# Kernel optimization log

Hardware: AMD Instinct MI355X
Metric: run time of the kernel (lower is better)

The kernel has to match this reference:

```python
import jax, jax.numpy as jnp
import numpy as np

N = 8192      # total nodes
B = 64        # graphs in batch
NPG = 128     # nodes per graph (equal-size graphs; idx sorted)
D_IN = 256
H = 256       # hidden_dim (d_model)
NH = 4        # nhead
HD = H // NH
FF = 2 * H    # dim_feedforward
NC = 16       # n_class


def setup_inputs() -> dict:
    key = jax.random.key(0)
    ks = jax.random.split(key, 16)
    def rn(k, shp, scale=0.05):
        return jax.random.normal(k, shp, jnp.float32) * scale
    inp = {}
    inp["x_in"] = jax.random.normal(ks[0], (N, D_IN), jnp.float32)
    # scale adjacency so each row sums ~1 to keep activations well-conditioned
    inp["adj"] = jax.random.uniform(ks[1], (N, N), jnp.float32) * (2.0 / N)
    inp["idx"] = jnp.repeat(jnp.arange(B, dtype=jnp.int32), NPG)
    inp["cum_nodes"] = jnp.full((B,), NPG, jnp.int32)
    # fc1
    inp["W1"] = rn(ks[2], (D_IN, H)); inp["b1"] = jnp.zeros((H,), jnp.float32)
    # transformer encoder layer (eval mode, dropout inactive)
    inp["in_w"] = rn(ks[3], (H, 3 * H)); inp["in_b"] = jnp.zeros((3 * H,), jnp.float32)
    inp["out_w"] = rn(ks[4], (H, H));    inp["out_b"] = jnp.zeros((H,), jnp.float32)
    inp["ln1_s"] = jnp.ones((H,), jnp.float32); inp["ln1_b"] = jnp.zeros((H,), jnp.float32)
    inp["ff1_w"] = rn(ks[5], (H, FF)); inp["ff1_b"] = jnp.zeros((FF,), jnp.float32)
    inp["ff2_w"] = rn(ks[6], (FF, H)); inp["ff2_b"] = jnp.zeros((H,), jnp.float32)
    inp["ln2_s"] = jnp.ones((H,), jnp.float32); inp["ln2_b"] = jnp.zeros((H,), jnp.float32)
    # fc3 / fc4
    inp["W3"] = rn(ks[7], (H, H));  inp["b3"] = jnp.zeros((H,), jnp.float32)
    inp["W4"] = rn(ks[8], (H, NC)); inp["b4"] = jnp.zeros((NC,), jnp.float32)
    return inp


def _layer_norm(x, s, b):
    mu = x.mean(-1, keepdims=True)
    xc = x - mu
    return xc * jax.lax.rsqrt((xc * xc).mean(-1, keepdims=True) + 1e-5) * s + b


def reference(x_in, adj, idx, cum_nodes, W1, b1, in_w, in_b, out_w, out_b,
              ln1_s, ln1_b, ff1_w, ff1_b, ff2_w, ff2_b, ln2_s, ln2_b,
              W3, b3, W4, b4):
    Bg = cum_nodes.shape[0]
    n = x_in.shape[0] // Bg  # equal-size graphs -> pad_sequence == reshape
    x = x_in @ W1 + b1                      # fc1
    x = jax.nn.relu(adj @ x)                # adjacency message passing
    p = x.reshape(Bg, n, H)                 # pack: idx is sorted, graphs equal size
    # --- TransformerEncoderLayer (post-LN, relu FFN, eval mode) ---
    qkv = p @ in_w + in_b                   # [B, n, 3H]
    q, k, v = jnp.split(qkv, 3, axis=-1)
    q = q.reshape(Bg, n, NH, HD); k = k.reshape(Bg, n, NH, HD); v = v.reshape(Bg, n, NH, HD)
    att = jax.nn.softmax(jnp.einsum('bqhd,bkhd->bhqk', q, k) / np.sqrt(HD), axis=-1)
    o = jnp.einsum('bhqk,bkhd->bqhd', att, v).reshape(Bg, n, H) @ out_w + out_b
    y = _layer_norm(p + o, ln1_s, ln1_b)
    ff = jax.nn.relu(y @ ff1_w + ff1_b) @ ff2_w + ff2_b
    y = _layer_norm(y + ff, ln2_s, ln2_b)
    # --- unpack + scatter-add pooling over graphs ---
    flat = y.reshape(Bg * n, H)
    pooled = jax.ops.segment_sum(flat, idx, num_segments=Bg)  # [B, H]
    out = jax.nn.relu(pooled @ W3 + b3) @ W4 + b4
    return jax.nn.log_softmax(out, axis=-1)
```

## Files before the change

### kernel.cpp

```cpp
#include <hip/hip_runtime.h>

typedef float fx4 __attribute__((ext_vector_type(4)));
typedef short s16x8 __attribute__((ext_vector_type(8)));
typedef short s16x4 __attribute__((ext_vector_type(4)));
typedef unsigned short ushort_t;

__device__ __forceinline__ short f2bf(float f) {
  union { float f; unsigned u; } v; v.f = f;
  unsigned r = v.u + 0x7FFFu + ((v.u >> 16) & 1u);
  return (short)(r >> 16);
}

__device__ __forceinline__ float bf2f(short h) {
  union { float f; unsigned u; } v;
  v.u = ((unsigned)(unsigned short)h) << 16;
  return v.f;
}

__device__ __forceinline__ unsigned cvt_pk_bf16(float a, float b) {
  unsigned r;
  asm("v_cvt_pk_bf16_f32 %0, %1, %2" : "=v"(r) : "v"(a), "v"(b));
  return r;
}

__device__ __forceinline__ s16x8 cvt8(fx4 a, fx4 b) {
  union { s16x8 s; unsigned u[4]; } w;
  w.u[0] = cvt_pk_bf16(a[0], a[1]);
  w.u[1] = cvt_pk_bf16(a[2], a[3]);
  w.u[2] = cvt_pk_bf16(b[0], b[1]);
  w.u[3] = cvt_pk_bf16(b[2], b[3]);
  return w.s;
}

__device__ __forceinline__ void gload16(const void* g, void* l) {
  __builtin_amdgcn_global_load_lds(
      (const __attribute__((address_space(1))) unsigned int*)g,
      (__attribute__((address_space(3))) unsigned int*)l, 16, 0, 0);
}

__global__ __launch_bounds__(256) void prep_kernel(
    const float* __restrict__ W1, const float* __restrict__ in_w,
    const float* __restrict__ out_w, const float* __restrict__ ff1_w,
    const float* __restrict__ ff2_w,
    ushort_t* __restrict__ W1t, ushort_t* __restrict__ in_wT,
    ushort_t* __restrict__ out_wT, ushort_t* __restrict__ ff1t,
    ushort_t* __restrict__ ff2t) {
  const int bid = blockIdx.x, t = threadIdx.x;
  const float* W; ushort_t* Wt; int K, N, base;
  if (bid < 256)       { W = W1;    Wt = W1t;    K = 256; N = 256; base = 0; }
  else if (bid < 1024) { W = in_w;  Wt = in_wT;  K = 256; N = 768; base = 256; }
  else if (bid < 1280) { W = out_w; Wt = out_wT; K = 256; N = 256; base = 1024; }
  else if (bid < 1792) { W = ff1_w; Wt = ff1t;   K = 256; N = 512; base = 1280; }
  else                 { W = ff2_w; Wt = ff2t;   K = 512; N = 256; base = 1792; }
  const int idx = (bid - base) * 256 + t;
  const int k = idx / N, n = idx - k * N;
  Wt[(size_t)n * K + k] = (ushort_t)f2bf(W[idx]);
}

template<int MF, bool AF32, int OUTM, bool RELU, bool RES>
__global__ __launch_bounds__(256) void gemm2(
    const void* __restrict__ Av, const ushort_t* __restrict__ Bt,
    const float* __restrict__ bias, const float* __restrict__ res,
    const float* __restrict__ lns, const float* __restrict__ lnb,
    float* __restrict__ Cf, ushort_t* __restrict__ Cb,
    int M, int N, int K, int kLen) {
  constexpr int BM = MF * 16;
  __shared__ __align__(16) ushort_t Asm[2][BM * 64];
  __shared__ __align__(16) ushort_t Bsm[256 * 64];
  const int t = threadIdx.x, lane = t & 63, wave = t >> 6;
  const int bm = blockIdx.y * BM;
  const int bn = blockIdx.x * 256;
  const int wn = wave * 64, fr = lane & 15, fq = lane >> 4;
  const int NT = kLen >> 6;
  const int x0 = ((fq) ^ (fr & 7)) * 8;
  const int x1 = ((4 + fq) ^ (fr & 7)) * 8;
  fx4 acc[MF][4] = {};

  const int gl = lane >> 3, gc = lane & 7;
  const int gsw = (gc ^ gl) * 8;
  const ushort_t* Bgl = Bt + (size_t)(bn + wave * 64 + gl) * K + gsw;
  const ushort_t* Agl =
      (const ushort_t*)Av + (size_t)(bm + wave * (BM / 4) + gl) * K + gsw;
  constexpr int TPR = 256 / BM;
  const int arow = t / TPR;
  const int ac0 = (t % TPR) * (BM / 4);
  const float* Afp = (const float*)Av + (size_t)(bm + arow) * K + ac0;
  fx4 R[MF / 2][2];

  auto issueB = [&](int kt) {
    #pragma unroll
    for (int i = 0; i < 8; ++i)
      gload16(Bgl + (size_t)i * 8 * K + kt * 64, &Bsm[wave * 4096 + i * 512]);
  };
  auto issueAg = [&](int buf, int kt) {
    #pragma unroll
    for (int i = 0; i < MF / 2; ++i)
      gload16(Agl + (size_t)i * 8 * K + kt * 64,
              &Asm[buf][wave * (BM * 16) + i * 512]);
  };
  auto loadR = [&](int kt) {
    #pragma unroll
    for (int w = 0; w < MF / 2; ++w) {
      R[w][0] = *(const fx4*)(Afp + kt * 64 + w * 8);
      R[w][1] = *(const fx4*)(Afp + kt * 64 + w * 8 + 4);
    }
  };
  auto writeA = [&](int buf) {
    #pragma unroll
    for (int w = 0; w < MF / 2; ++w) {
      const int cs = ((ac0 >> 3) + w) ^ (arow & 7);
      *(s16x8*)&Asm[buf][arow * 64 + cs * 8] = cvt8(R[w][0], R[w][1]);
    }
  };

  if constexpr (AF32) { loadR(0); issueB(0); writeA(0); loadR(1); }
  else { issueAg(0, 0); issueB(0); }
  __syncthreads();

  #pragma unroll 1
  for (int kt = 0; kt < NT; ++kt) {
    const int cur = kt & 1;
    s16x8 b0[4], b1[4], a0[MF], a1[MF];
    #pragma unroll
    for (int nf = 0; nf < 4; ++nf) {
      b0[nf] = *(const s16x8*)&Bsm[(wn + nf * 16 + fr) * 64 + x0];
      b1[nf] = *(const s16x8*)&Bsm[(wn + nf * 16 + fr) * 64 + x1];
    }
    #pragma unroll
    for (int mf = 0; mf < MF; ++mf)
      a0[mf] = *(const s16x8*)&Asm[cur][(mf * 16 + fr) * 64 + x0];
    asm volatile("s_waitcnt lgkmcnt(0)" ::: "memory");
    if (kt + 1 < NT) {
      if constexpr (AF32) {
        writeA(cur ^ 1);
        if (kt + 2 < NT) loadR(kt + 2);
        issueB(kt + 1);
      } else {
        issueAg(cur ^ 1, kt + 1);
        issueB(kt + 1);
      }
    }
    #pragma unroll
    for (int mf = 0; mf < MF; ++mf)
      #pragma unroll
      for (int nf = 0; nf < 4; ++nf)
        acc[mf][nf] = __builtin_amdgcn_mfma_f32_16x16x32_bf16(
            a0[mf], b0[nf], acc[mf][nf], 0, 0, 0);
    #pragma unroll
    for (int mf = 0; mf < MF; ++mf)
      a1[mf] = *(const s16x8*)&Asm[cur][(mf * 16 + fr) * 64 + x1];
    #pragma unroll
    for (int mf = 0; mf < MF; ++mf)
      #pragma unroll
      for (int nf = 0; nf < 4; ++nf)
        acc[mf][nf] = __builtin_amdgcn_mfma_f32_16x16x32_bf16(
            a1[mf], b1[nf], acc[mf][nf], 0, 0, 0);
    __syncthreads();
  }

  if constexpr (OUTM == 3) {
    #pragma unroll
    for (int mf = 0; mf < MF; ++mf)
      #pragma unroll
      for (int nf = 0; nf < 4; ++nf) {
        const int col = bn + wn + nf * 16 + fr;
        const float bb = bias[col];
        s16x4 w;
        #pragma unroll
        for (int r = 0; r < 4; ++r) w[r] = f2bf(acc[mf][nf][r] + bb);
        *(s16x4*)&Cb[(size_t)col * M + bm + mf * 16 + fq * 4] = w;
      }
  } else {
    #pragma unroll
    for (int mf = 0; mf < MF; ++mf)
      #pragma unroll
      for (int nf = 0; nf < 4; ++nf) {
        const int col = bn + wn + nf * 16 + fr;
        const float bb = bias[col];
        #pragma unroll
        for (int r = 0; r < 4; ++r) {
          const int row = bm + mf * 16 + fq * 4 + r;
          float x = acc[mf][nf][r] + bb;
          if constexpr (RES) x += res[(size_t)row * N + col];
          if constexpr (RELU) x = fmaxf(x, 0.f);
          if constexpr (OUTM == 0 || OUTM == 2) Cf[(size_t)row * N + col] = x;
          if constexpr (OUTM == 1 || OUTM == 2)
            Cb[(size_t)row * N + col] = (ushort_t)f2bf(x);
        }
      }
  }
}

__global__ __launch_bounds__(256) void adjmm6(
    const float* __restrict__ adj, const ushort_t* __restrict__ xT,
    ushort_t* __restrict__ part) {
  constexpr int NT = 16;
  __shared__ __align__(16) ushort_t Asm[2][128 * 64];
  __shared__ __align__(16) ushort_t Bsm[256 * 64];
  const int t = threadIdx.x, lane = t & 63, wave = t >> 6;
  const int kh = blockIdx.x, bm = blockIdx.y * 128;
  const int kOff = kh * 1024;
  const int wn = wave * 64, fr = lane & 15, fq = lane >> 4;
  const int x0 = (fq ^ (fr & 7)) * 8, x1 = ((4 + fq) ^ (fr & 7)) * 8;
  const int gl = lane >> 3, gsw = ((lane & 7) ^ gl) * 8;

  const ushort_t* Bgl = xT + (size_t)(wn + gl) * 8192 + kOff + gsw;
  const int arow = t >> 1;
  const int alane = t & 1;
  const float* Afp = adj + (size_t)(bm + arow) * 8192 + kOff;

  fx4 R[8];
  auto loadR = [&](int kt) {
    #pragma unroll
    for (int j = 0; j < 8; ++j)
      R[j] = *(const fx4*)(Afp + kt * 64 + alane * 4 + j * 8);
  };
  auto writeA = [&](int buf) {
    #pragma unroll
    for (int j = 0; j < 8; ++j) {
      union { s16x4 s; unsigned u[2]; } w;
      w.u[0] = cvt_pk_bf16(R[j][0], R[j][1]);
      w.u[1] = cvt_pk_bf16(R[j][2], R[j][3]);
      *(s16x4*)&Asm[buf][arow * 64 + (j ^ (arow & 7)) * 8 + alane * 4] = w.s;
    }
  };
  auto issueB = [&](int kt) {
    #pragma unroll
    for (int i = 0; i < 8; ++i)
      gload16(Bgl + (size_t)i * 8 * 8192 + kt * 64,
              &Bsm[wave * 4096 + i * 512]);
  };

  fx4 acc[8][4] = {};
  loadR(0);
  issueB(0);
  writeA(0);
  loadR(1);
  asm volatile("s_waitcnt lgkmcnt(0)" ::: "memory");
  asm volatile("s_waitcnt vmcnt(8)" ::: "memory");
  __builtin_amdgcn_sched_barrier(0);
  __builtin_amdgcn_s_barrier();
  __builtin_amdgcn_sched_barrier(0);

  #pragma unroll 1
  for (int kt = 0; kt < NT; ++kt) {
    const int cur = kt & 1;
    s16x8 b0[4], b1[4], a[8];
    #pragma unroll
    for (int nf = 0; nf < 4; ++nf) {
      b0[nf] = *(const s16x8*)&Bsm[(wn + nf * 16 + fr) * 64 + x0];
      b1[nf] = *(const s16x8*)&Bsm[(wn + nf * 16 + fr) * 64 + x1];
    }
    #pragma unroll
    for (int mf = 0; mf < 8; ++mf)
      a[mf] = *(const s16x8*)&Asm[cur][(mf * 16 + fr) * 64 + x0];
    asm volatile("s_waitcnt lgkmcnt(0)" ::: "memory");
    __builtin_amdgcn_sched_barrier(0);
    if (kt + 1 < NT) {
      issueB(kt + 1);
      writeA(cur ^ 1);
      if (kt + 2 < NT) loadR(kt + 2);
    }
    #pragma unroll
    for (int mf = 0; mf < 8; ++mf)
      #pragma unroll
      for (int nf = 0; nf < 4; ++nf)
        acc[mf][nf] = __builtin_amdgcn_mfma_f32_16x16x32_bf16(
            a[mf], b0[nf], acc[mf][nf], 0, 0, 0);
    #pragma unroll
    for (int mf = 0; mf < 8; ++mf)
      a[mf] = *(const s16x8*)&Asm[cur][(mf * 16 + fr) * 64 + x1];
    #pragma unroll
    for (int mf = 0; mf < 8; ++mf)
      #pragma unroll
      for (int nf = 0; nf < 4; ++nf)
        acc[mf][nf] = __builtin_amdgcn_mfma_f32_16x16x32_bf16(
            a[mf], b1[nf], acc[mf][nf], 0, 0, 0);
    if (kt + 1 < NT) {
      asm volatile("s_waitcnt lgkmcnt(0)" ::: "memory");
      if (kt + 2 < NT)
        asm volatile("s_waitcnt vmcnt(8)" ::: "memory");
      else
        asm volatile("s_waitcnt vmcnt(0)" ::: "memory");
      __builtin_amdgcn_sched_barrier(0);
      __builtin_amdgcn_s_barrier();
      __builtin_amdgcn_sched_barrier(0);
    }
  }

  ushort_t* po = part + (size_t)kh * (8192ull * 256ull);
  #pragma unroll
  for (int mf = 0; mf < 8; ++mf)
    #pragma unroll
    for (int nf = 0; nf < 4; ++nf)
      #pragma unroll
      for (int r = 0; r < 4; ++r)
        po[(size_t)(bm + mf * 16 + fq * 4 + r) * 256 + wn + nf * 16 + fr] =
            (ushort_t)f2bf(acc[mf][nf][r]);
}

__global__ __launch_bounds__(256) void relu_reduce8(
    const ushort_t* __restrict__ part, float* __restrict__ p,
    ushort_t* __restrict__ pb) {
  const size_t i = ((size_t)blockIdx.x * 256 + threadIdx.x) * 8;
  const size_t S = 8192ull * 256ull;
  float a[8] = {};
  #pragma unroll
  for (int j = 0; j < 8; ++j) {
    const s16x8 v = *(const s16x8*)(part + j * S + i);
    #pragma unroll
    for (int c = 0; c < 8; ++c) a[c] += bf2f(v[c]);
  }
  fx4 v0, v1;
  #pragma unroll
  for (int c = 0; c < 4; ++c) {
    v0[c] = fmaxf(a[c], 0.f);
    v1[c] = fmaxf(a[c + 4], 0.f);
  }
  *(fx4*)(p + i) = v0;
  *(fx4*)(p + i + 4) = v1;
  s16x8 w;
  #pragma unroll
  for (int c = 0; c < 4; ++c) { w[c] = f2bf(v0[c]); w[c + 4] = f2bf(v1[c]); }
  *(s16x8*)(pb + i) = w;
}

__global__ __launch_bounds__(256) void att_fused(
    const ushort_t* __restrict__ qkv, ushort_t* __restrict__ attout) {
  __shared__ float k_s[128][68];
  __shared__ float v_s[128][68];
  __shared__ float s_s[128][129];
  __shared__ float pm[2][128];
  __shared__ float ps[2][128];
  const int bh = blockIdx.x, b = bh >> 2, h = bh & 3;
  const int t = threadIdx.x;
  const ushort_t* qb = qkv + (size_t)b * 128 * 768 + h * 64;
  for (int u = t; u < 1024; u += 256) {
    const int n = u >> 3, d8 = (u & 7) * 8;
    const s16x8 kk = *(const s16x8*)(qb + (size_t)n * 768 + 256 + d8);
    const s16x8 vv = *(const s16x8*)(qb + (size_t)n * 768 + 512 + d8);
    #pragma unroll
    for (int c = 0; c < 8; ++c) {
      k_s[n][d8 + c] = bf2f(kk[c]);
      v_s[n][d8 + c] = bf2f(vv[c]);
    }
  }
  const int row = t & 127, kh = t >> 7;
  fx4 qr[16];
  {
    const s16x8* q8 = (const s16x8*)(qb + (size_t)row * 768);
    #pragma unroll
    for (int j = 0; j < 8; ++j) {
      const s16x8 qv = q8[j];
      qr[2*j][0] = bf2f(qv[0]); qr[2*j][1] = bf2f(qv[1]);
      qr[2*j][2] = bf2f(qv[2]); qr[2*j][3] = bf2f(qv[3]);
      qr[2*j+1][0] = bf2f(qv[4]); qr[2*j+1][1] = bf2f(qv[5]);
      qr[2*j+1][2] = bf2f(qv[6]); qr[2*j+1][3] = bf2f(qv[7]);
    }
  }
  __syncthreads();
  float m = -1e30f;
  for (int j = 0; j < 64; ++j) {
    const int jj = kh * 64 + j;
    const fx4* kr = (const fx4*)&k_s[jj][0];
    float s0 = 0.f, s1 = 0.f, s2 = 0.f, s3 = 0.f;
    #pragma unroll
    for (int c = 0; c < 16; c += 4) {
      fx4 k0 = kr[c], k1 = kr[c + 1], k2 = kr[c + 2], k3 = kr[c + 3];
      s0 += qr[c][0]*k0[0] + qr[c][1]*k0[1] + qr[c][2]*k0[2] + qr[c][3]*k0[3];
      s1 += qr[c+1][0]*k1[0] + qr[c+1][1]*k1[1] + qr[c+1][2]*k1[2] + qr[c+1][3]*k1[3];
      s2 += qr[c+2][0]*k2[0] + qr[c+2][1]*k2[1] + qr[c+2][2]*k2[2] + qr[c+2][3]*k2[3];
      s3 += qr[c+3][0]*k3[0] + qr[c+3][1]*k3[1] + qr[c+3][2]*k3[2] + qr[c+3][3]*k3[3];
    }
    const float s = (s0 + s1 + s2 + s3) * 0.125f;
    s_s[row][jj] = s;
    m = fmaxf(m, s);
  }
  pm[kh][row] = m;
  __syncthreads();
  const float m2 = fmaxf(pm[0][row], pm[1][row]);
  float sum = 0.f;
  for (int j = 0; j < 64; ++j) {
    const int jj = kh * 64 + j;
    const float e = __expf(s_s[row][jj] - m2);
    s_s[row][jj] = e;
    sum += e;
  }
  ps[kh][row] = sum;
  __syncthreads();
  const int row2 = t >> 1, dh = (t & 1) * 32;
  const float inv = 1.f / (ps[0][row2] + ps[1][row2]);
  fx4 acc4[8] = {};
  for (int k = 0; k < 128; ++k) {
    const float e = s_s[row2][k];
    const fx4* vr = (const fx4*)&v_s[k][dh];
    #pragma unroll
    for (int c = 0; c < 8; ++c) acc4[c] += e * vr[c];
  }
  ushort_t* orow = attout + (size_t)(b * 128 + row2) * 256 + h * 64 + dh;
  #pragma unroll
  for (int c = 0; c < 8; ++c) {
    const fx4 v = acc4[c] * inv;
    s16x4 w;
    #pragma unroll
    for (int j = 0; j < 4; ++j) w[j] = f2bf(v[j]);
    *(s16x4*)(orow + c * 4) = w;
  }
}

__global__ __launch_bounds__(256) void tail_kernel(
    const ushort_t* __restrict__ attout, const ushort_t* __restrict__ out_wT,
    const float* __restrict__ out_b, const float* __restrict__ p_res,
    const float* __restrict__ ln1_s, const float* __restrict__ ln1_b,
    const ushort_t* __restrict__ ff1t, const float* __restrict__ ff1_b,
    const ushort_t* __restrict__ ff2t, const float* __restrict__ ff2_b,
    const float* __restrict__ ln2_s, const float* __restrict__ ln2_b,
    float* __restrict__ pooled4) {
  __shared__ __align__(16) ushort_t Asm[2][32 * 64];
  __shared__ __align__(16) ushort_t Bsm[256 * 64];
  __shared__ __align__(16) ushort_t y_s[32 * 256];
  __shared__ __align__(16) ushort_t f1_s[32 * 512];
  __shared__ float red_s[128], red_q[128];
  const int t = threadIdx.x, lane = t & 63, wave = t >> 6;
  const int bq = blockIdx.x, bm = bq * 32;
  const int wn = wave * 64, fr = lane & 15, fq = lane >> 4;
  const int x0 = (fq ^ (fr & 7)) * 8, x1 = ((4 + fq) ^ (fr & 7)) * 8;
  const int gl = lane >> 3, gc = lane & 7, gsw = (gc ^ gl) * 8;

  fx4 acc[2][4] = {};
  {
    const ushort_t* Agl = attout + (size_t)(bm + wave * 8 + gl) * 256 + gsw;
    const ushort_t* Bgl = out_wT + (size_t)(wave * 64 + gl) * 256 + gsw;
    auto issueA = [&](int buf, int kt) {
      gload16(Agl + kt * 64, &Asm[buf][wave * 512]);
    };
    auto issueB = [&](int kt) {
      #pragma unroll
      for (int i = 0; i < 8; ++i)
        gload16(Bgl + (size_t)i * 8 * 256 + kt * 64,
                &Bsm[wave * 4096 + i * 512]);
    };
    issueA(0, 0); issueB(0);
    __syncthreads();
    #pragma unroll 1
    for (int kt = 0; kt < 4; ++kt) {
      const int cur = kt & 1;
      s16x8 b0[4], b1[4], a0[2], a1[2];
      #pragma unroll
      for (int nf = 0; nf < 4; ++nf) {
        b0[nf] = *(const s16x8*)&Bsm[(wn + nf * 16 + fr) * 64 + x0];
        b1[nf] = *(const s16x8*)&Bsm[(wn + nf * 16 + fr) * 64 + x1];
      }
      #pragma unroll
      for (int mf = 0; mf < 2; ++mf) {
        a0[mf] = *(const s16x8*)&Asm[cur][(mf * 16 + fr) * 64 + x0];
        a1[mf] = *(const s16x8*)&Asm[cur][(mf * 16 + fr) * 64 + x1];
      }
      asm volatile("s_waitcnt lgkmcnt(0)" ::: "memory");
      if (kt < 3) { issueA(cur ^ 1, kt + 1); issueB(kt + 1); }
      #pragma unroll
      for (int mf = 0; mf < 2; ++mf)
        #pragma unroll
        for (int nf = 0; nf < 4; ++nf) {
          acc[mf][nf] = __builtin_amdgcn_mfma_f32_16x16x32_bf16(
              a0[mf], b0[nf], acc[mf][nf], 0, 0, 0);
          acc[mf][nf] = __builtin_amdgcn_mfma_f32_16x16x32_bf16(
              a1[mf], b1[nf], acc[mf][nf], 0, 0, 0);
        }
      __syncthreads();
    }
  }
  float yv[2][4][4];
  #pragma unroll
  for (int mf = 0; mf < 2; ++mf)
    #pragma unroll
    for (int nf = 0; nf < 4; ++nf) {
      const int col = wn + nf * 16 + fr;
      #pragma unroll
      for (int r = 0; r < 4; ++r) {
        const int row = bm + mf * 16 + fq * 4 + r;
        yv[mf][nf][r] = acc[mf][nf][r] + out_b[col] +
                        p_res[(size_t)row * 256 + col];
      }
    }
  {
    #pragma unroll
    for (int mf = 0; mf < 2; ++mf)
      #pragma unroll
      for (int r = 0; r < 4; ++r) {
        float s = yv[mf][0][r] + yv[mf][1][r] + yv[mf][2][r] + yv[mf][3][r];
        float q = yv[mf][0][r]*yv[mf][0][r] + yv[mf][1][r]*yv[mf][1][r] +
                  yv[mf][2][r]*yv[mf][2][r] + yv[mf][3][r]*yv[mf][3][r];
        #pragma unroll
        for (int off = 1; off < 16; off <<= 1) {
          s += __shfl_xor(s, off, 64);
          q += __shfl_xor(q, off, 64);
        }
        if (fr == 0) {
          red_s[(mf * 16 + fq * 4 + r) * 4 + wave] = s;
          red_q[(mf * 16 + fq * 4 + r) * 4 + wave] = q;
        }
      }
    __syncthreads();
    #pragma unroll
    for (int mf = 0; mf < 2; ++mf)
      #pragma unroll
      for (int r = 0; r < 4; ++r) {
        const int rl = mf * 16 + fq * 4 + r;
        const float st = red_s[rl*4] + red_s[rl*4+1] + red_s[rl*4+2] + red_s[rl*4+3];
        const float qt = red_q[rl*4] + red_q[rl*4+1] + red_q[rl*4+2] + red_q[rl*4+3];
        const float mu = st * (1.f / 256.f);
        const float rr = rsqrtf(qt * (1.f / 256.f) - mu * mu + 1e-5f);
        #pragma unroll
        for (int nf = 0; nf < 4; ++nf) {
          const int col = wn + nf * 16 + fr;
          const float o = (yv[mf][nf][r] - mu) * rr * ln1_s[col] + ln1_b[col];
          yv[mf][nf][r] = o;
          y_s[rl * 256 + ((col >> 3) ^ (rl & 7)) * 8 + (col & 7)] =
              (ushort_t)f2bf(o);
        }
      }
  }
  __syncthreads();

  #pragma unroll 1
  for (int ng = 0; ng < 2; ++ng) {
    const ushort_t* Bgl = ff1t + (size_t)(ng * 256 + wave * 64 + gl) * 256 + gsw;
    auto issueB = [&](int kt) {
      #pragma unroll
      for (int i = 0; i < 8; ++i)
        gload16(Bgl + (size_t)i * 8 * 256 + kt * 64,
                &Bsm[wave * 4096 + i * 512]);
    };
    fx4 a2[2][4] = {};
    issueB(0);
    #pragma unroll 1
    for (int kt = 0; kt < 4; ++kt) {
      asm volatile("s_waitcnt vmcnt(0)" ::: "memory");
      s16x8 b0[4], b1[4], a0[2], a1[2];
      #pragma unroll
      for (int nf = 0; nf < 4; ++nf) {
        b0[nf] = *(const s16x8*)&Bsm[(wn + nf * 16 + fr) * 64 + x0];
        b1[nf] = *(const s16x8*)&Bsm[(wn + nf * 16 + fr) * 64 + x1];
      }
      #pragma unroll
      for (int mf = 0; mf < 2; ++mf) {
        const int row = mf * 16 + fr;
        a0[mf] = *(const s16x8*)&y_s[row * 256 + ((kt*8 + fq) ^ (row & 7)) * 8];
        a1[mf] = *(const s16x8*)&y_s[row * 256 + ((kt*8 + 4 + fq) ^ (row & 7)) * 8];
      }
      asm volatile("s_waitcnt lgkmcnt(0)" ::: "memory");
      if (kt < 3) issueB(kt + 1);
      #pragma unroll
      for (int mf = 0; mf < 2; ++mf)
        #pragma unroll
        for (int nf = 0; nf < 4; ++nf) {
          a2[mf][nf] = __builtin_amdgcn_mfma_f32_16x16x32_bf16(
              a0[mf], b0[nf], a2[mf][nf], 0, 0, 0);
          a2[mf][nf] = __builtin_amdgcn_mfma_f32_16x16x32_bf16(
              a1[mf], b1[nf], a2[mf][nf], 0, 0, 0);
        }
    }
    #pragma unroll
    for (int mf = 0; mf < 2; ++mf)
      #pragma unroll
      for (int nf = 0; nf < 4; ++nf) {
        const int col = ng * 256 + wn + nf * 16 + fr;
        const float bb = ff1_b[col];
        #pragma unroll
        for (int r = 0; r < 4; ++r) {
          const int rl = mf * 16 + fq * 4 + r;
          const float x = fmaxf(a2[mf][nf][r] + bb, 0.f);
          f1_s[rl * 512 + ((col >> 3) ^ (rl & 7)) * 8 + (col & 7)] =
              (ushort_t)f2bf(x);
        }
      }
  }
  __syncthreads();

  {
    const ushort_t* Bgl = ff2t + (size_t)(wave * 64 + gl) * 512 + gsw;
    auto issueB = [&](int kt) {
      #pragma unroll
      for (int i = 0; i < 8; ++i)
        gload16(Bgl + (size_t)i * 8 * 512 + kt * 64,
                &Bsm[wave * 4096 + i * 512]);
    };
    fx4 a3[2][4] = {};
    issueB(0);
    #pragma unroll 1
    for (int kt = 0; kt < 8; ++kt) {
      asm volatile("s_waitcnt vmcnt(0)" ::: "memory");
      s16x8 b0[4], b1[4], a0[2], a1[2];
      #pragma unroll
      for (int nf = 0; nf < 4; ++nf) {
        b0[nf] = *(const s16x8*)&Bsm[(wn + nf * 16 + fr) * 64 + x0];
        b1[nf] = *(const s16x8*)&Bsm[(wn + nf * 16 + fr) * 64 + x1];
      }
      #pragma unroll
      for (int mf = 0; mf < 2; ++mf) {
        const int row = mf * 16 + fr;
        a0[mf] = *(const s16x8*)&f1_s[row * 512 + ((kt*8 + fq) ^ (row & 7)) * 8];
        a1[mf] = *(const s16x8*)&f1_s[row * 512 + ((kt*8 + 4 + fq) ^ (row & 7)) * 8];
      }
      asm volatile("s_waitcnt lgkmcnt(0)" ::: "memory");
      if (kt < 7) issueB(kt + 1);
      #pragma unroll
      for (int mf = 0; mf < 2; ++mf)
        #pragma unroll
        for (int nf = 0; nf < 4; ++nf) {
          a3[mf][nf] = __builtin_amdgcn_mfma_f32_16x16x32_bf16(
              a0[mf], b0[nf], a3[mf][nf], 0, 0, 0);
          a3[mf][nf] = __builtin_amdgcn_mfma_f32_16x16x32_bf16(
              a1[mf], b1[nf], a3[mf][nf], 0, 0, 0);
        }
    }
    float vv[2][4][4];
    #pragma unroll
    for (int mf = 0; mf < 2; ++mf)
      #pragma unroll
      for (int nf = 0; nf < 4; ++nf) {
        const int col = wn + nf * 16 + fr;
        const float bb = ff2_b[col];
        #pragma unroll
        for (int r = 0; r < 4; ++r)
          vv[mf][nf][r] = a3[mf][nf][r] + bb + yv[mf][nf][r];
      }
    __syncthreads();
    #pragma unroll
    for (int mf = 0; mf < 2; ++mf)
      #pragma unroll
      for (int r = 0; r < 4; ++r) {
        float s = vv[mf][0][r] + vv[mf][1][r] + vv[mf][2][r] + vv[mf][3][r];
        float q = vv[mf][0][r]*vv[mf][0][r] + vv[mf][1][r]*vv[mf][1][r] +
                  vv[mf][2][r]*vv[mf][2][r] + vv[mf][3][r]*vv[mf][3][r];
        #pragma unroll
        for (int off = 1; off < 16; off <<= 1) {
          s += __shfl_xor(s, off, 64);
          q += __shfl_xor(q, off, 64);
        }
        if (fr == 0) {
          red_s[(mf * 16 + fq * 4 + r) * 4 + wave] = s;
          red_q[(mf * 16 + fq * 4 + r) * 4 + wave] = q;
        }
      }
    __syncthreads();
    float colsum[4] = {};
    #pragma unroll
    for (int mf = 0; mf < 2; ++mf)
      #pragma unroll
      for (int r = 0; r < 4; ++r) {
        const int rl = mf * 16 + fq * 4 + r;
        const float st = red_s[rl*4] + red_s[rl*4+1] + red_s[rl*4+2] + red_s[rl*4+3];
        const float qt = red_q[rl*4] + red_q[rl*4+1] + red_q[rl*4+2] + red_q[rl*4+3];
        const float mu = st * (1.f / 256.f);
        const float rr = rsqrtf(qt * (1.f / 256.f) - mu * mu + 1e-5f);
        #pragma unroll
        for (int nf = 0; nf < 4; ++nf) {
          const int col = wn + nf * 16 + fr;
          colsum[nf] += (vv[mf][nf][r] - mu) * rr * ln2_s[col] + ln2_b[col];
        }
      }
    #pragma unroll
    for (int nf = 0; nf < 4; ++nf) {
      colsum[nf] += __shfl_xor(colsum[nf], 16, 64);
      colsum[nf] += __shfl_xor(colsum[nf], 32, 64);
    }
    if (lane < 16)
      #pragma unroll
      for (int nf = 0; nf < 4; ++nf)
        pooled4[(size_t)bq * 256 + wn + nf * 16 + fr] = colsum[nf];
  }
}

__global__ __launch_bounds__(256) void head_kernel(
    const float* __restrict__ pooled4, const float* __restrict__ W3,
    const float* __restrict__ b3, const float* __restrict__ W4,
    const float* __restrict__ b4, float* __restrict__ out) {
  __shared__ float sp[256];
  __shared__ float t1[256];
  __shared__ float logits[16];
  const int b = blockIdx.x, h = threadIdx.x;
  sp[h] = pooled4[(size_t)(b * 4 + 0) * 256 + h] +
          pooled4[(size_t)(b * 4 + 1) * 256 + h] +
          pooled4[(size_t)(b * 4 + 2) * 256 + h] +
          pooled4[(size_t)(b * 4 + 3) * 256 + h];
  __syncthreads();
  float a = b3[h];
  for (int k = 0; k < 256; ++k) a += sp[k] * W3[k * 256 + h];
  t1[h] = fmaxf(a, 0.f);
  __syncthreads();
  if (h < 16) {
    float o = b4[h];
    for (int j = 0; j < 256; ++j) o += t1[j] * W4[j * 16 + h];
    logits[h] = o;
  }
  __syncthreads();
  if (h < 16) {
    float mm = -1e30f;
    #pragma unroll
    for (int c = 0; c < 16; ++c) mm = fmaxf(mm, logits[c]);
    float se = 0.f;
    #pragma unroll
    for (int c = 0; c < 16; ++c) se += __expf(logits[c] - mm);
    out[b * 16 + h] = logits[h] - mm - logf(se);
  }
}

extern "C" void kernel_launch(void* const* d_in, const int* in_sizes, int n_in,
                              void* d_out, int out_size, void* d_ws, size_t ws_size,
                              hipStream_t stream) {
  const float* x_in  = (const float*)d_in[0];
  const float* adj   = (const float*)d_in[1];
  const float* W1    = (const float*)d_in[4];
  const float* b1    = (const float*)d_in[5];
  const float* in_w  = (const float*)d_in[6];
  const float* in_b  = (const float*)d_in[7];
  const float* out_w = (const float*)d_in[8];
  const float* out_b = (const float*)d_in[9];
  const float* ln1_s = (const float*)d_in[10];
  const float* ln1_b = (const float*)d_in[11];
  const float* ff1_w = (const float*)d_in[12];
  const float* ff1_b = (const float*)d_in[13];
  const float* ff2_w = (const float*)d_in[14];
  const float* ff2_b = (const float*)d_in[15];
  const float* ln2_s = (const float*)d_in[16];
  const float* ln2_b = (const float*)d_in[17];
  const float* W3    = (const float*)d_in[18];
  const float* b3    = (const float*)d_in[19];
  const float* W4    = (const float*)d_in[20];
  const float* b4    = (const float*)d_in[21];
  char* ws = (char*)d_ws;
  const size_t MB = 1ull << 20;
  ushort_t* xT      = (ushort_t*)(ws);
  ushort_t* W1t     = (ushort_t*)(ws + 4 * MB);
  ushort_t* in_wT   = (ushort_t*)(ws + 4 * MB + 131072);
  ushort_t* out_wT  = (ushort_t*)(ws + 4 * MB + 524288);
  ushort_t* ff1t    = (ushort_t*)(ws + 4 * MB + 655360);
  ushort_t* ff2t    = (ushort_t*)(ws + 4 * MB + 917504);
  float*    p       = (float*)(ws + 8 * MB);
  ushort_t* p_bf    = (ushort_t*)(ws + 16 * MB);
  ushort_t* qkv_bf  = (ushort_t*)(ws + 20 * MB);
  ushort_t* attout  = (ushort_t*)(ws + 32 * MB);
  float*    pooled4 = (float*)(ws + 36 * MB);
  ushort_t* part    = (ushort_t*)(ws + 37 * MB);
  float*    outp    = (float*)d_out;
  (void)in_sizes; (void)n_in; (void)out_size; (void)ws_size;

  prep_kernel<<<2304, 256, 0, stream>>>(W1, in_w, out_w, ff1_w, ff2_w,
                                        W1t, in_wT, out_wT, ff1t, ff2t);
  gemm2<2, true, 3, false, false><<<dim3(1, 256), 256, 0, stream>>>(
      x_in, W1t, b1, nullptr, nullptr, nullptr, nullptr, xT,
      8192, 256, 256, 256);
  adjmm6<<<dim3(8, 64), 256, 0, stream>>>(adj, xT, part);
  relu_reduce8<<<1024, 256, 0, stream>>>(part, p, p_bf);
  gemm2<4, false, 1, false, false><<<dim3(3, 128), 256, 0, stream>>>(
      p_bf, in_wT, in_b, nullptr, nullptr, nullptr, nullptr, qkv_bf,
      8192, 768, 256, 256);
  att_fused<<<256, 256, 0, stream>>>(qkv_bf, attout);
  tail_kernel<<<256, 256, 0, stream>>>(
      attout, out_wT, out_b, p, ln1_s, ln1_b, ff1t, ff1_b,
      ff2t, ff2_b, ln2_s, ln2_b, pooled4);
  head_kernel<<<64, 256, 0, stream>>>(pooled4, W3, b3, W4, b4, outp);
}
```

Baseline: 197.6 us.

## Split adjacency GEMM over output columns and halve split-K with B double-buffering

The adjacency matmul now tiles the 256 output columns into two 128-wide blocks and uses 4 K-splits instead of 8, with each block covering twice the K range. The xT operand tile is double-buffered and prefetched two steps ahead, and the partial-sum reduction reads 4 partials instead of 8. This cuts split-K partial traffic and reduction work, but every fp32 adjacency tile is now loaded and converted by two blocks, which can raise DRAM traffic on the dominant input.

```diff
diff --git a/kernel.cpp b/kernel.cpp
--- a/kernel.cpp
+++ b/kernel.cpp
@@ -191,20 +191,20 @@
   }
 }
 
-__global__ __launch_bounds__(256) void adjmm6(
+__global__ __launch_bounds__(256) void adjmm7(
     const float* __restrict__ adj, const ushort_t* __restrict__ xT,
     ushort_t* __restrict__ part) {
-  constexpr int NT = 16;
+  constexpr int NT = 32;
   __shared__ __align__(16) ushort_t Asm[2][128 * 64];
-  __shared__ __align__(16) ushort_t Bsm[256 * 64];
+  __shared__ __align__(16) ushort_t Bsm[2][128 * 64];
   const int t = threadIdx.x, lane = t & 63, wave = t >> 6;
-  const int kh = blockIdx.x, bm = blockIdx.y * 128;
-  const int kOff = kh * 1024;
-  const int wn = wave * 64, fr = lane & 15, fq = lane >> 4;
+  const int kh = blockIdx.x, bm = blockIdx.y * 128, bn = blockIdx.z * 128;
+  const int kOff = kh * 2048;
+  const int wn = wave * 32, fr = lane & 15, fq = lane >> 4;
   const int x0 = (fq ^ (fr & 7)) * 8, x1 = ((4 + fq) ^ (fr & 7)) * 8;
   const int gl = lane >> 3, gsw = ((lane & 7) ^ gl) * 8;
 
-  const ushort_t* Bgl = xT + (size_t)(wn + gl) * 8192 + kOff + gsw;
+  const ushort_t* Bgl = xT + (size_t)(bn + wn + gl) * 8192 + kOff + gsw;
   const int arow = t >> 1;
   const int alane = t & 1;
   const float* Afp = adj + (size_t)(bm + arow) * 8192 + kOff;
@@ -224,16 +224,16 @@
       *(s16x4*)&Asm[buf][arow * 64 + (j ^ (arow & 7)) * 8 + alane * 4] = w.s;
     }
   };
-  auto issueB = [&](int kt) {
-    #pragma unroll
-    for (int i = 0; i < 8; ++i)
+  auto issueB = [&](int buf, int kt) {
+    #pragma unroll
+    for (int i = 0; i < 4; ++i)
       gload16(Bgl + (size_t)i * 8 * 8192 + kt * 64,
-              &Bsm[wave * 4096 + i * 512]);
+              &Bsm[buf][wave * 2048 + i * 512]);
   };
 
-  fx4 acc[8][4] = {};
+  fx4 acc[8][2] = {};
   loadR(0);
-  issueB(0);
+  issueB(0, 0);
   writeA(0);
   loadR(1);
   asm volatile("s_waitcnt lgkmcnt(0)" ::: "memory");
@@ -241,72 +241,69 @@
   __builtin_amdgcn_sched_barrier(0);
   __builtin_amdgcn_s_barrier();
   __builtin_amdgcn_sched_barrier(0);
+  issueB(1, 1);
 
   #pragma unroll 1
   for (int kt = 0; kt < NT; ++kt) {
     const int cur = kt & 1;
-    s16x8 b0[4], b1[4], a[8];
-    #pragma unroll
-    for (int nf = 0; nf < 4; ++nf) {
-      b0[nf] = *(const s16x8*)&Bsm[(wn + nf * 16 + fr) * 64 + x0];
-      b1[nf] = *(const s16x8*)&Bsm[(wn + nf * 16 + fr) * 64 + x1];
+    s16x8 a0[8], b0[2], b1[2];
+    #pragma unroll
+    for (int nf = 0; nf < 2; ++nf) {
+      b0[nf] = *(const s16x8*)&Bsm[cur][(wn + nf * 16 + fr) * 64 + x0];
+      b1[nf] = *(const s16x8*)&Bsm[cur][(wn + nf * 16 + fr) * 64 + x1];
     }
     #pragma unroll
     for (int mf = 0; mf < 8; ++mf)
-      a[mf] = *(const s16x8*)&Asm[cur][(mf * 16 + fr) * 64 + x0];
-    asm volatile("s_waitcnt lgkmcnt(0)" ::: "memory");
-    __builtin_amdgcn_sched_barrier(0);
+      a0[mf] = *(const s16x8*)&Asm[cur][(mf * 16 + fr) * 64 + x0];
     if (kt + 1 < NT) {
-      issueB(kt + 1);
       writeA(cur ^ 1);
       if (kt + 2 < NT) loadR(kt + 2);
     }
     #pragma unroll
     for (int mf = 0; mf < 8; ++mf)
       #pragma unroll
-      for (int nf = 0; nf < 4; ++nf)
+      for (int nf = 0; nf < 2; ++nf)
         acc[mf][nf] = __builtin_amdgcn_mfma_f32_16x16x32_bf16(
-            a[mf], b0[nf], acc[mf][nf], 0, 0, 0);
+            a0[mf], b0[nf], acc[mf][nf], 0, 0, 0);
     #pragma unroll
     for (int mf = 0; mf < 8; ++mf)
-      a[mf] = *(const s16x8*)&Asm[cur][(mf * 16 + fr) * 64 + x1];
+      a0[mf] = *(const s16x8*)&Asm[cur][(mf * 16 + fr) * 64 + x1];
     #pragma unroll
     for (int mf = 0; mf < 8; ++mf)
       #pragma unroll
-      for (int nf = 0; nf < 4; ++nf)
+      for (int nf = 0; nf < 2; ++nf)
         acc[mf][nf] = __builtin_amdgcn_mfma_f32_16x16x32_bf16(
-            a[mf], b1[nf], acc[mf][nf], 0, 0, 0);
-    if (kt + 1 < NT) {
-      asm volatile("s_waitcnt lgkmcnt(0)" ::: "memory");
-      if (kt + 2 < NT)
-        asm volatile("s_waitcnt vmcnt(8)" ::: "memory");
-      else
-        asm volatile("s_waitcnt vmcnt(0)" ::: "memory");
-      __builtin_amdgcn_sched_barrier(0);
-      __builtin_amdgcn_s_barrier();
-      __builtin_amdgcn_sched_barrier(0);
-    }
+            a0[mf], b1[nf], acc[mf][nf], 0, 0, 0);
+    asm volatile("s_waitcnt lgkmcnt(0)" ::: "memory");
+    if (kt + 2 < NT)
+      asm volatile("s_waitcnt vmcnt(8)" ::: "memory");
+    else
+      asm volatile("s_waitcnt vmcnt(0)" ::: "memory");
+    __builtin_amdgcn_sched_barrier(0);
+    __builtin_amdgcn_s_barrier();
+    __builtin_amdgcn_sched_barrier(0);
+    if (kt + 2 < NT) issueB(cur, kt + 2);
   }
 
   ushort_t* po = part + (size_t)kh * (8192ull * 256ull);
   #pragma unroll
   for (int mf = 0; mf < 8; ++mf)
     #pragma unroll
-    for (int nf = 0; nf < 4; ++nf)
+    for (int nf = 0; nf < 2; ++nf)
       #pragma unroll
       for (int r = 0; r < 4; ++r)
-        po[(size_t)(bm + mf * 16 + fq * 4 + r) * 256 + wn + nf * 16 + fr] =
+        po[(size_t)(bm + mf * 16 + fq * 4 + r) * 256 + bn + wn + nf * 16 + fr] =
             (ushort_t)f2bf(acc[mf][nf][r]);
 }
 
-__global__ __launch_bounds__(256) void relu_reduce8(
+__global__ __launch_bounds__(256) void relu_reduce4(
     const ushort_t* __restrict__ part, float* __restrict__ p,
     ushort_t* __restrict__ pb) {
   const size_t i = ((size_t)blockIdx.x * 256 + threadIdx.x) * 8;
   const size_t S = 8192ull * 256ull;
   float a[8] = {};
   #pragma unroll
-  for (int j = 0; j < 8; ++j) {
+  for (int j = 0; j < 4; ++j) {
     const s16x8 v = *(const s16x8*)(part + j * S + i);
     #pragma unroll
     for (int c = 0; c < 8; ++c) a[c] += bf2f(v[c]);
@@ -752,8 +749,8 @@
   gemm2<2, true, 3, false, false><<<dim3(1, 256), 256, 0, stream>>>(
       x_in, W1t, b1, nullptr, nullptr, nullptr, nullptr, xT,
       8192, 256, 256, 256);
-  adjmm6<<<dim3(8, 64), 256, 0, stream>>>(adj, xT, part);
-  relu_reduce8<<<1024, 256, 0, stream>>>(part, p, p_bf);
+  adjmm7<<<dim3(4, 64, 2), 256, 0, stream>>>(adj, xT, part);
+  relu_reduce4<<<1024, 256, 0, stream>>>(part, p, p_bf);
   gemm2<4, false, 1, false, false><<<dim3(3, 128), 256, 0, stream>>>(
       p_bf, in_wT, in_b, nullptr, nullptr, nullptr, nullptr, qkv_bf,
       8192, 768, 256, 256);
```

After: 201.5 us. No clear change (+2.0%).
